# Kernel optimization log

Measured on AMD Instinct MI355X. Metric: run time of the kernel, lower is better.

## Reference

```python
import jax, jax.numpy as jnp
import numpy as np

B, N, E, H = 4, 4096, 1024, 16
D = E // H


def setup_inputs() -> dict:
    key = jax.random.key(0)
    ks = jax.random.split(key, 8)
    s = 1.0 / np.sqrt(E)
    x = jax.random.normal(ks[0], (B, N, E), dtype=jnp.float32)
    # binary multiplicative sparsity pattern over the head-head score matrix
    sparsity_pattern = jax.random.randint(ks[1], (H, H), 0, 2).astype(jnp.float32)
    Wq = jax.random.normal(ks[2], (E, E), dtype=jnp.float32) * s
    bq = jax.random.normal(ks[3], (E,), dtype=jnp.float32) * s
    Wk = jax.random.normal(ks[4], (E, E), dtype=jnp.float32) * s
    bk = jax.random.normal(ks[5], (E,), dtype=jnp.float32) * s
    Wv = jax.random.normal(ks[6], (E, E), dtype=jnp.float32) * s
    bv = jax.random.normal(ks[7], (E,), dtype=jnp.float32) * s
    return {"x": x, "sparsity_pattern": sparsity_pattern,
            "Wq": Wq, "bq": bq, "Wk": Wk, "bk": bk, "Wv": Wv, "bv": bv}


def reference(x, sparsity_pattern, Wq, bq, Wk, bk, Wv, bv):
    b, n, e = x.shape
    # torch Linear: y = x @ W.T + b
    q = (x @ Wq.T + bq).reshape(b, n, H, D)
    k = (x @ Wk.T + bk).reshape(b, n, H, D)
    v = (x @ Wv.T + bv).reshape(b, n, H, D)
    # torch.matmul over last two dims of [B,N,H,D]: scores are [B,N,H,H]
    scores = jnp.einsum('bnhd,bngd->bnhg', q, k) * sparsity_pattern
    attn = jax.nn.softmax(scores, axis=-1)
    out = jnp.einsum('bnhg,bngd->bnhd', attn, v).reshape(b, n, e)
    return out
```

## Files before the change

kernel.cpp:

```cpp
#include <hip/hip_runtime.h>
#include <hip/hip_bf16.h>

#define M_   16384
#define K_   1024
#define NQKV 3072

typedef _Float16 f16x4 __attribute__((ext_vector_type(4)));
typedef _Float16 f16x8 __attribute__((ext_vector_type(8)));
typedef float    f32x4 __attribute__((ext_vector_type(4)));

__global__ __launch_bounds__(256) void cvt_f32_f16(const float* __restrict__ in,
                                                   _Float16* __restrict__ o, int n4) {
  int i = blockIdx.x * blockDim.x + threadIdx.x;
  const int stride = gridDim.x * blockDim.x;
  for (; i < n4; i += stride) {
    float4 v = ((const float4*)in)[i];
    f16x4 h; h[0] = (_Float16)v.x; h[1] = (_Float16)v.y;
    h[2] = (_Float16)v.z; h[3] = (_Float16)v.w;
    *(f16x4*)&o[(size_t)i * 4] = h;
  }
}

__global__ __launch_bounds__(512, 2) void gemm_qkv(
    const _Float16* __restrict__ xh, const _Float16* __restrict__ wh,
    const float* __restrict__ bq, const float* __restrict__ bk,
    const float* __restrict__ bv, _Float16* __restrict__ qkv)
{
  __shared__ __align__(16) _Float16 As[2][256 * 64];
  __shared__ __align__(16) _Float16 Bs[2][256 * 64];

  const int tid  = threadIdx.x;
  const int ln   = tid & 63;
  const int w    = tid >> 6;
  const int wm2  = w >> 2;
  const int wn4  = w & 3;
  const int lcol = ln & 15, quad = ln >> 4;

  const int bid = blockIdx.x;
  const int swz = (bid & 7) * 96 + (bid >> 3);
  const int m0 = (swz / 12) * 256;
  const int n0 = (swz % 12) * 256;

  f32x4 acc[8][4];
#pragma unroll
  for (int i = 0; i < 8; ++i)
#pragma unroll
    for (int j = 0; j < 4; ++j) acc[i][j] = f32x4{0.f, 0.f, 0.f, 0.f};

#define STAGE(BUF, T)                                                          \
  {                                                                            \
    const int k0s = (T) * 64;                                                  \
    _Pragma("unroll")                                                          \
    for (int i = 0; i < 4; ++i) {                                              \
      const int c  = i * 512 + tid;                                            \
      const int r  = c >> 3;                                                   \
      const int cb = (c & 7) ^ (r & 7);                                        \
      const int db = (i * 512 + w * 64) * 8;       \
      __builtin_amdgcn_global_load_lds(                                        \
          (const __attribute__((address_space(1))) void*)(                     \
              xh + (size_t)(m0 + r) * K_ + k0s + cb * 8),                      \
          (__attribute__((address_space(3))) void*)(&As[BUF][db]), 16, 0, 0);  \
      __builtin_amdgcn_global_load_lds(                                        \
          (const __attribute__((address_space(1))) void*)(                     \
              wh + (size_t)(n0 + r) * K_ + k0s + cb * 8),                      \
          (__attribute__((address_space(3))) void*)(&Bs[BUF][db]), 16, 0, 0);  \
    }                                                                          \
  }

  f16x8 a[4][2], b[2][2];

#define LOADA(MH)                                                              \
  _Pragma("unroll")                                                            \
  for (int mi = 0; mi < 4; ++mi) {                                             \
    const int ar = wm2 * 128 + (MH) * 64 + mi * 16 + lcol;                     \
    const int sw = ar & 7;                                                     \
    a[mi][0] = *(const f16x8*)&As[cur][ar * 64 + ((quad    ) ^ sw) * 8];       \
    a[mi][1] = *(const f16x8*)&As[cur][ar * 64 + ((quad + 4) ^ sw) * 8];       \
  }

#define LOADB(NH)                                                              \
  _Pragma("unroll")                                                            \
  for (int ni = 0; ni < 2; ++ni) {                                             \
    const int br = wn4 * 64 + (NH) * 32 + ni * 16 + lcol;                      \
    const int sw = br & 7;                                                     \
    b[ni][0] = *(const f16x8*)&Bs[cur][br * 64 + ((quad    ) ^ sw) * 8];       \
    b[ni][1] = *(const f16x8*)&Bs[cur][br * 64 + ((quad + 4) ^ sw) * 8];       \
  }

#define MFMA16(MH, NH)                                                         \
  __builtin_amdgcn_s_setprio(1);                                               \
  _Pragma("unroll")                                                            \
  for (int kb = 0; kb < 2; ++kb)                                               \
    _Pragma("unroll")                                                          \
    for (int mi = 0; mi < 4; ++mi)                                             \
      _Pragma("unroll")                                                        \
      for (int ni = 0; ni < 2; ++ni)                                           \
        acc[(MH) * 4 + mi][(NH) * 2 + ni] =                                    \
            __builtin_amdgcn_mfma_f32_16x16x32_f16(                            \
                a[mi][kb], b[ni][kb], acc[(MH) * 4 + mi][(NH) * 2 + ni],       \
                0, 0, 0);                                                      \
  __builtin_amdgcn_s_setprio(0);

  STAGE(0, 0);
  asm volatile("s_waitcnt vmcnt(0)" ::: "memory");
  __builtin_amdgcn_s_barrier();

  for (int t = 0; t < 16; ++t) {
    const int cur = t & 1;
    if (t < 15) STAGE(cur ^ 1, t + 1);

    LOADA(0); LOADB(0); MFMA16(0, 0);
    __builtin_amdgcn_s_barrier(); __builtin_amdgcn_sched_barrier(0);
    LOADA(1);           MFMA16(1, 0);
    __builtin_amdgcn_s_barrier(); __builtin_amdgcn_sched_barrier(0);
              LOADB(1); MFMA16(1, 1);
    __builtin_amdgcn_s_barrier(); __builtin_amdgcn_sched_barrier(0);
    LOADA(0);           MFMA16(0, 1);
    if (t < 15) asm volatile("s_waitcnt vmcnt(0)" ::: "memory");
    __builtin_amdgcn_s_barrier(); __builtin_amdgcn_sched_barrier(0);
  }

#pragma unroll
  for (int nh = 0; nh < 4; ++nh) {
    const int col = n0 + wn4 * 64 + nh * 16 + lcol;
    const int seg = col >> 10, cs = col & 1023;
    const float bi = ((seg == 0) ? bq : (seg == 1) ? bk : bv)[cs];
#pragma unroll
    for (int mi = 0; mi < 8; ++mi) {
      const int r0 = m0 + wm2 * 128 + mi * 16 + quad * 4;
#pragma unroll
      for (int r = 0; r < 4; ++r)
        qkv[(size_t)(r0 + r) * 3072 + col] = (_Float16)(acc[mi][nh][r] + bi);
    }
  }
#undef STAGE
#undef LOADA
#undef LOADB
#undef MFMA16
}

__global__ __launch_bounds__(256) void attn_kernel(
    const _Float16* __restrict__ qkv,
    const float* __restrict__ pat,
    float* __restrict__ out)
{
  __shared__ float pat_s[256];
  __shared__ __align__(16) _Float16 Ps[4][16 * 24];
  __shared__ __align__(16) _Float16 Vt[4][64 * 24];

  const int tid  = threadIdx.x;
  const int ln   = tid & 63;
  const int wv   = tid >> 6;
  const int lcol = ln & 15, quad = ln >> 4;
  const int t    = blockIdx.x * 4 + wv;

  pat_s[tid] = pat[tid];
  __syncthreads();

  const _Float16* qg = qkv + (size_t)t * 3072;
  const _Float16* kg = qg + 1024;
  const _Float16* vg = qg + 2048;

#pragma unroll
  for (int i = 0; i < 2; i++) {
    const int e = i * 64 + ln;
    const int g = e >> 3, c = (e & 7) * 8;
    f16x8 vc = *(const f16x8*)(vg + g * 64 + c);
#pragma unroll
    for (int j = 0; j < 8; j++) Vt[wv][(c + j) * 24 + g] = vc[j];
  }

  f16x8 aq0 = *(const f16x8*)(qg + lcol * 64 + quad * 8);
  f16x8 aq1 = *(const f16x8*)(qg + lcol * 64 + 32 + quad * 8);
  f16x8 bk0 = *(const f16x8*)(kg + lcol * 64 + quad * 8);
  f16x8 bk1 = *(const f16x8*)(kg + lcol * 64 + 32 + quad * 8);
  f32x4 s = {0.f, 0.f, 0.f, 0.f};
  s = __builtin_amdgcn_mfma_f32_16x16x32_f16(aq0, bk0, s, 0, 0, 0);
  s = __builtin_amdgcn_mfma_f32_16x16x32_f16(aq1, bk1, s, 0, 0, 0);

#pragma unroll
  for (int r = 0; r < 4; r++) {
    const float sv = s[r] * pat_s[(quad * 4 + r) * 16 + lcol];
    float m = sv;
#pragma unroll
    for (int msk = 1; msk < 16; msk <<= 1) m = fmaxf(m, __shfl_xor(m, msk, 64));
    const float e = __expf(sv - m);
    float su = e;
#pragma unroll
    for (int msk = 1; msk < 16; msk <<= 1) su += __shfl_xor(su, msk, 64);
    Ps[wv][(quad * 4 + r) * 24 + lcol] = (_Float16)(e / su);
  }

  f16x8 ap = {};
  if (quad < 2) ap = *(const f16x8*)&Ps[wv][lcol * 24 + quad * 8];

  f32x4 o[4];
#pragma unroll
  for (int dt = 0; dt < 4; dt++) {
    f16x8 bvf = {};
    if (quad < 2) bvf = *(const f16x8*)&Vt[wv][(dt * 16 + lcol) * 24 + quad * 8];
    f32x4 z = {0.f, 0.f, 0.f, 0.f};
    o[dt] = __builtin_amdgcn_mfma_f32_16x16x32_f16(ap, bvf, z, 0, 0, 0);
  }

  float* op = out + (size_t)t * 1024;
#pragma unroll
  for (int dt = 0; dt < 4; dt++)
#pragma unroll
    for (int r = 0; r < 4; r++)
      op[(quad * 4 + r) * 64 + dt * 16 + lcol] = o[dt][r];
}

extern "C" void kernel_launch(void* const* d_in, const int* in_sizes, int n_in,
                              void* d_out, int out_size, void* d_ws, size_t ws_size,
                              hipStream_t stream) {
  const float* x   = (const float*)d_in[0];
  const float* pat = (const float*)d_in[1];
  const float* Wq  = (const float*)d_in[2];
  const float* bq  = (const float*)d_in[3];
  const float* Wk  = (const float*)d_in[4];
  const float* bk  = (const float*)d_in[5];
  const float* Wv  = (const float*)d_in[6];
  const float* bv  = (const float*)d_in[7];

  _Float16* qkvh = (_Float16*)d_ws;
  _Float16* xh   = qkvh + (size_t)50331648;
  _Float16* wh   = qkvh + (size_t)67108864;

  cvt_f32_f16<<<4096, 256, 0, stream>>>(x,  xh,               4194304);
  cvt_f32_f16<<<1024, 256, 0, stream>>>(Wq, wh,                262144);
  cvt_f32_f16<<<1024, 256, 0, stream>>>(Wk, wh + 1048576,      262144);
  cvt_f32_f16<<<1024, 256, 0, stream>>>(Wv, wh + 2097152,      262144);

  gemm_qkv<<<768, 512, 0, stream>>>(xh, wh, bq, bk, bv, qkvh);
  attn_kernel<<<M_ / 4, 256, 0, stream>>>(qkvh, pat, (float*)d_out);
}
```

Before: 292.3 us.

## Stream GEMM tiles in quarter-chunks with finer-grained prefetch and merge weight conversions

After: 283.5 us. 3.0% less time.

```diff
diff --git a/kernel.cpp b/kernel.cpp
--- a/kernel.cpp
+++ b/kernel.cpp
@@ -21,6 +21,21 @@
   }
 }
 
+__global__ __launch_bounds__(256) void cvt3_f32_f16(
+    const float* __restrict__ a, const float* __restrict__ b,
+    const float* __restrict__ c, _Float16* __restrict__ o, int n4each) {
+  const float* src = (blockIdx.y == 0) ? a : (blockIdx.y == 1) ? b : c;
+  _Float16* dst = o + (size_t)blockIdx.y * n4each * 4;
+  int i = blockIdx.x * blockDim.x + threadIdx.x;
+  const int stride = gridDim.x * blockDim.x;
+  for (; i < n4each; i += stride) {
+    float4 v = ((const float4*)src)[i];
+    f16x4 h; h[0] = (_Float16)v.x; h[1] = (_Float16)v.y;
+    h[2] = (_Float16)v.z; h[3] = (_Float16)v.w;
+    *(f16x4*)&dst[(size_t)i * 4] = h;
+  }
+}
+
 __global__ __launch_bounds__(512, 2) void gemm_qkv(
     const _Float16* __restrict__ xh, const _Float16* __restrict__ wh,
     const float* __restrict__ bq, const float* __restrict__ bk,
@@ -47,44 +62,56 @@
 #pragma unroll
     for (int j = 0; j < 4; ++j) acc[i][j] = f32x4{0.f, 0.f, 0.f, 0.f};
 
-#define STAGE(BUF, T)                                                          \
-  {                                                                            \
-    const int k0s = (T) * 64;                                                  \
-    _Pragma("unroll")                                                          \
-    for (int i = 0; i < 4; ++i) {                                              \
-      const int c  = i * 512 + tid;                                            \
-      const int r  = c >> 3;                                                   \
-      const int cb = (c & 7) ^ (r & 7);                                        \
-      const int db = (i * 512 + w * 64) * 8;       \
+  f16x8 a[4][2], b[2][2];
+
+#define STAGE_A(BUF, KT, X)                                                    \
+  { _Pragma("unroll")                                                          \
+    for (int j = 0; j < 2; ++j) {                                              \
+      const int c   = j * 512 + tid;                                           \
+      const int rr  = c >> 3;                                                  \
+      const int r   = (X) * 64 + (rr & 63) + ((rr >> 6) << 7);                 \
+      const int cb  = (c & 7) ^ (r & 7);                                       \
+      const int rr0 = j * 64 + w * 8;                                          \
+      const int r0  = (X) * 64 + (rr0 & 63) + ((rr0 >> 6) << 7);               \
       __builtin_amdgcn_global_load_lds(                                        \
           (const __attribute__((address_space(1))) void*)(                     \
-              xh + (size_t)(m0 + r) * K_ + k0s + cb * 8),                      \
-          (__attribute__((address_space(3))) void*)(&As[BUF][db]), 16, 0, 0);  \
+              xh + (size_t)(m0 + r) * K_ + (KT) * 64 + cb * 8),                \
+          (__attribute__((address_space(3))) void*)(&As[BUF][r0 * 64]),        \
+          16, 0, 0);                                                           \
+    } }
+
+#define STAGE_B(BUF, KT, Y)                                                    \
+  { _Pragma("unroll")                                                          \
+    for (int j = 0; j < 2; ++j) {                                              \
+      const int c   = j * 512 + tid;                                           \
+      const int rr  = c >> 3;                                                  \
+      const int r   = ((rr >> 5) << 6) + (Y) * 32 + (rr & 31);                 \
+      const int cb  = (c & 7) ^ (r & 7);                                       \
+      const int rr0 = j * 64 + w * 8;                                          \
+      const int r0  = ((rr0 >> 5) << 6) + (Y) * 32 + (rr0 & 31);               \
       __builtin_amdgcn_global_load_lds(                                        \
           (const __attribute__((address_space(1))) void*)(                     \
-              wh + (size_t)(n0 + r) * K_ + k0s + cb * 8),                      \
-          (__attribute__((address_space(3))) void*)(&Bs[BUF][db]), 16, 0, 0);  \
-    }                                                                          \
-  }
-
-  f16x8 a[4][2], b[2][2];
-
-#define LOADA(MH)                                                              \
+              wh + (size_t)(n0 + r) * K_ + (KT) * 64 + cb * 8),                \
+          (__attribute__((address_space(3))) void*)(&Bs[BUF][r0 * 64]),        \
+          16, 0, 0);                                                           \
+    } }
+
+#define LOADA(BUF, MH)                                                         \
   _Pragma("unroll")                                                            \
   for (int mi = 0; mi < 4; ++mi) {                                             \
     const int ar = wm2 * 128 + (MH) * 64 + mi * 16 + lcol;                     \
     const int sw = ar & 7;                                                     \
-    a[mi][0] = *(const f16x8*)&As[cur][ar * 64 + ((quad    ) ^ sw) * 8];       \
-    a[mi][1] = *(const f16x8*)&As[cur][ar * 64 + ((quad + 4) ^ sw) * 8];       \
-  }
-
-#define LOADB(NH)                                                              \
+    a[mi][0] = *(const f16x8*)&As[BUF][ar * 64 + ((quad    ) ^ sw) * 8];       \
+    a[mi][1] = *(const f16x8*)&As[BUF][ar * 64 + ((quad + 4) ^ sw) * 8];       \
+  }
+
+#define LOADB(BUF, NH)                                                         \
   _Pragma("unroll")                                                            \
   for (int ni = 0; ni < 2; ++ni) {                                             \
     const int br = wn4 * 64 + (NH) * 32 + ni * 16 + lcol;                      \
     const int sw = br & 7;                                                     \
-    b[ni][0] = *(const f16x8*)&Bs[cur][br * 64 + ((quad    ) ^ sw) * 8];       \
-    b[ni][1] = *(const f16x8*)&Bs[cur][br * 64 + ((quad + 4) ^ sw) * 8];       \
+    b[ni][0] = *(const f16x8*)&Bs[BUF][br * 64 + ((quad    ) ^ sw) * 8];       \
+    b[ni][1] = *(const f16x8*)&Bs[BUF][br * 64 + ((quad + 4) ^ sw) * 8];       \
   }
 
 #define MFMA16(MH, NH)                                                         \
@@ -101,24 +128,47 @@
                 0, 0, 0);                                                      \
   __builtin_amdgcn_s_setprio(0);
 
-  STAGE(0, 0);
-  asm volatile("s_waitcnt vmcnt(0)" ::: "memory");
-  __builtin_amdgcn_s_barrier();
-
-  for (int t = 0; t < 16; ++t) {
-    const int cur = t & 1;
-    if (t < 15) STAGE(cur ^ 1, t + 1);
-
-    LOADA(0); LOADB(0); MFMA16(0, 0);
-    __builtin_amdgcn_s_barrier(); __builtin_amdgcn_sched_barrier(0);
-    LOADA(1);           MFMA16(1, 0);
-    __builtin_amdgcn_s_barrier(); __builtin_amdgcn_sched_barrier(0);
-              LOADB(1); MFMA16(1, 1);
-    __builtin_amdgcn_s_barrier(); __builtin_amdgcn_sched_barrier(0);
-    LOADA(0);           MFMA16(0, 1);
-    if (t < 15) asm volatile("s_waitcnt vmcnt(0)" ::: "memory");
-    __builtin_amdgcn_s_barrier(); __builtin_amdgcn_sched_barrier(0);
-  }
+#define BAR()  { __builtin_amdgcn_s_barrier(); __builtin_amdgcn_sched_barrier(0); }
+#define LGKM0() { asm volatile("s_waitcnt lgkmcnt(0)" ::: "memory");           \
+                  __builtin_amdgcn_sched_barrier(0); }
+#define VM6() asm volatile("s_waitcnt vmcnt(6)" ::: "memory")
+#define VM0() asm volatile("s_waitcnt vmcnt(0)" ::: "memory")
+
+#define GITER(KT0, LAST)                                                       \
+  {                                                                   \
+    LOADA(0, 0); LOADB(0, 0); STAGE_A(1, (KT0) + 1, 0);                        \
+    BAR(); LGKM0(); MFMA16(0, 0); BAR();                                       \
+                                                                      \
+    LOADA(0, 1); if (!(LAST)) STAGE_B(0, (KT0) + 2, 0);                        \
+    BAR(); LGKM0(); MFMA16(1, 0); BAR();                                       \
+                                                                      \
+    LOADB(0, 1); if (!(LAST)) STAGE_A(0, (KT0) + 2, 1);                        \
+    BAR(); LGKM0(); MFMA16(1, 1); BAR();                                       \
+                                                                      \
+    LOADA(0, 0); if (!(LAST)) STAGE_B(0, (KT0) + 2, 1);                        \
+    if (LAST) { VM0(); } else { VM6(); }                                       \
+    BAR(); LGKM0(); MFMA16(0, 1); BAR();                                       \
+                                                                      \
+    LOADA(1, 0); LOADB(1, 0); if (!(LAST)) STAGE_A(0, (KT0) + 2, 0);           \
+    BAR(); LGKM0(); MFMA16(0, 0); BAR();                                       \
+                                                                      \
+    LOADA(1, 1); if (!(LAST)) STAGE_B(1, (KT0) + 3, 0);                        \
+    BAR(); LGKM0(); MFMA16(1, 0); BAR();                                       \
+                                                                      \
+    LOADB(1, 1); if (!(LAST)) STAGE_A(1, (KT0) + 3, 1);                        \
+    BAR(); LGKM0(); MFMA16(1, 1); BAR();                                       \
+                                                                      \
+    LOADA(1, 0); if (!(LAST)) { STAGE_B(1, (KT0) + 3, 1); VM6(); }             \
+    BAR(); LGKM0(); MFMA16(0, 1); BAR();                                       \
+  }
+
+  STAGE_A(0, 0, 0); STAGE_B(0, 0, 0); STAGE_A(0, 0, 1); STAGE_B(0, 0, 1);
+  STAGE_B(1, 1, 0); STAGE_A(1, 1, 1); STAGE_B(1, 1, 1);
+  VM6(); BAR();
+
+#pragma unroll 1
+  for (int it = 0; it < 7; ++it) { GITER(it * 2, 0); }
+  GITER(14, 1);
 
 #pragma unroll
   for (int nh = 0; nh < 4; ++nh) {
@@ -133,10 +183,16 @@
         qkv[(size_t)(r0 + r) * 3072 + col] = (_Float16)(acc[mi][nh][r] + bi);
     }
   }
-#undef STAGE
+#undef STAGE_A
+#undef STAGE_B
 #undef LOADA
 #undef LOADB
 #undef MFMA16
+#undef BAR
+#undef LGKM0
+#undef VM6
+#undef VM0
+#undef GITER
 }
 
 __global__ __launch_bounds__(256) void attn_kernel(
@@ -227,10 +283,8 @@
   _Float16* xh   = qkvh + (size_t)50331648;
   _Float16* wh   = qkvh + (size_t)67108864;
 
-  cvt_f32_f16<<<4096, 256, 0, stream>>>(x,  xh,               4194304);
-  cvt_f32_f16<<<1024, 256, 0, stream>>>(Wq, wh,                262144);
-  cvt_f32_f16<<<1024, 256, 0, stream>>>(Wk, wh + 1048576,      262144);
-  cvt_f32_f16<<<1024, 256, 0, stream>>>(Wv, wh + 2097152,      262144);
+  cvt_f32_f16<<<4096, 256, 0, stream>>>(x, xh, 4194304);
+  cvt3_f32_f16<<<dim3(256, 3), 256, 0, stream>>>(Wq, Wk, Wv, wh, 262144);
 
   gemm_qkv<<<768, 512, 0, stream>>>(xh, wh, bq, bk, bv, qkvh);
   attn_kernel<<<M_ / 4, 256, 0, stream>>>(qkvh, pat, (float*)d_out);
```
